# Kernel optimization log

Hardware: AMD Instinct MI355X
Metric: run time of the kernel (lower is better)

The kernel has to match this reference:

```python
import jax, jax.numpy as jnp
import numpy as np
from jax import lax

N_C = 2
T = 5
NE = 17   # equality constraints per (sample, t)
NV = 24   # variables per (sample, t): p(4), f(4), f_e(4), alpha1(2), alpha2(2), gamma(4), gamma_e(4)
ITERS = 400
B = 512

F_MASK = jnp.zeros((NV,), bool).at[4:8].set(True)     # L1-penalized coords (f)
NN_MASK = jnp.zeros((NV,), bool).at[12:24].set(True)  # nonneg coords (alpha1, alpha2, gamma, gamma_e)


def _conv(x, w, b):
    return lax.conv_general_dilated(x, w, (1, 1), 'VALID',
                                    dimension_numbers=('NCHW', 'OIHW', 'NCHW')) + b[None, :, None, None]


def _maxpool(x, k):
    return lax.reduce_window(x, -jnp.inf, lax.max, (1, 1, k, k), (1, 1, k, k), 'VALID')


def _encoder(img, cw1, cb1, cw2, cb2, w3, b3, w4, b4):
    h = jax.nn.relu(_maxpool(_conv(img, cw1, cb1), 2))   # (B,10,20,20)
    h = jax.nn.relu(_maxpool(_conv(h, cw2, cb2), 4))     # (B,20,4,4)
    h = h.reshape(h.shape[0], -1)                        # (B,320)
    h = jax.nn.relu(h @ w3.T + b3)                       # dropout is eval-mode identity
    return jax.nn.relu(h @ w4.T + b4)                    # (B,100)


def _mlp(h, w1, b1, w2, b2, w3, b3):
    h = jax.nn.relu(h @ w1.T + b1)  # dropout eval-mode identity
    h = jax.nn.relu(h @ w2.T + b2)
    return h @ w3.T + b3


def _build_Ab(r, ddr, fc, p_e, fc_e, v, p_r):
    # one (t)-slice: r(3), ddr(3), fc(8), p_e(4), fc_e(8), v(8), p_r(4) -> A(17,24), b(17)
    A = jnp.zeros((NE, NV))
    b = jnp.zeros((NE,))
    # force balance x: sum(f) + f_e0 + f_e1 = ddr0  (original f[:20] covers all 4 rows, f[20:] empty)
    A = A.at[0, 4:8].set(1.0).at[0, 8].set(1.0).at[0, 9].set(1.0)
    b = b.at[0].set(ddr[0])
    # force balance y: f_e2 + f_e3 = ddr1
    A = A.at[1, 10].set(1.0).at[1, 11].set(1.0)
    b = b.at[1].set(ddr[1])
    # torque balance
    A = A.at[2, 6].set(p_r[0] - r[0]).at[2, 4].set(-(p_r[2] - r[1]))
    A = A.at[2, 7].set(p_r[1] - r[0]).at[2, 5].set(-(p_r[3] - r[1]))
    A = A.at[2, 10].set(p_e[0] - r[0]).at[2, 8].set(-(p_e[2] - r[1]))
    A = A.at[2, 11].set(p_e[1] - r[0]).at[2, 9].set(-(p_e[3] - r[1]))
    b = b.at[2].set(ddr[2])
    for c in range(N_C):
        # p = alpha1*v_a + alpha2*v_b, alpha1+alpha2=1
        A = A.at[3 + 3 * c, c].set(1.0).at[3 + 3 * c, 12 + c].set(-v[2 * c]).at[3 + 3 * c, 14 + c].set(-v[2 * c + 2])
        A = A.at[4 + 3 * c, c + 2].set(1.0).at[4 + 3 * c, 12 + c].set(-v[2 * c + 1]).at[4 + 3 * c, 14 + c].set(-v[2 * c + 3])
        A = A.at[5 + 3 * c, 12 + c].set(1.0).at[5 + 3 * c, 14 + c].set(1.0)
        b = b.at[5 + 3 * c].set(1.0)
        # friction cone: f = gamma1*fc_a + gamma2*fc_b
        A = A.at[9 + 2 * c, 16 + c].set(fc[2 * c]).at[9 + 2 * c, 18 + c].set(fc[2 * c + 2]).at[9 + 2 * c, 4 + c].set(-1.0)
        A = A.at[10 + 2 * c, 16 + c].set(fc[2 * c + 1]).at[10 + 2 * c, 18 + c].set(fc[2 * c + 3]).at[10 + 2 * c, 6 + c].set(-1.0)
    # external force cones
    A = A.at[13, 20].set(fc_e[0]).at[13, 21].set(fc_e[2]).at[13, 8].set(-1.0)
    A = A.at[14, 20].set(fc_e[1]).at[14, 21].set(fc_e[3]).at[14, 10].set(-1.0)
    A = A.at[15, 22].set(fc_e[4]).at[15, 23].set(fc_e[6]).at[15, 9].set(-1.0)
    A = A.at[16, 22].set(fc_e[5]).at[16, 23].set(fc_e[7]).at[16, 11].set(-1.0)
    return A, b


def _specnorm(A):
    def body(i, u):
        u = A.T @ (A @ u)
        return u / (jnp.linalg.norm(u) + 1e-12)
    u = lax.fori_loop(0, 25, body, jnp.ones((A.shape[-1],), A.dtype))
    return jnp.linalg.norm(A @ u)


def _solve_lp(A, b):
    # batched: min ||f||_1  s.t.  A z = b,  z[nn] >= 0   via PDHG (Chambolle-Pock)
    P = A.shape[0]
    L = lax.stop_gradient(jax.vmap(_specnorm)(A))
    tau = (0.9 / (L + 1e-8))[:, None]
    sig = tau

    def step(carry, _):
        z, zb, y = carry
        y = y + sig * (jnp.einsum('pev,pv->pe', A, zb) - b)
        g = z - tau * jnp.einsum('pev,pe->pv', A, y)
        zn = jnp.where(F_MASK, jnp.sign(g) * jnp.maximum(jnp.abs(g) - tau, 0.0),
                       jnp.where(NN_MASK, jnp.maximum(g, 0.0), g))
        return (zn, 2.0 * zn - z, y), None

    z0 = jnp.zeros((P, NV))
    y0 = jnp.zeros((P, NE))
    (z, _, _), _ = lax.scan(step, (z0, z0, y0), None, length=ITERS)
    return z


def reference(xtraj, x, x_img, cw1, cb1, cw2, cb2, w3, b3, w4, b4,
              pw1, pb1, pw2, pb2, pw3, pb3, vw1, vb1, vw2, vb2, vw3, vb3):
    Bn = xtraj.shape[0]
    img = x_img.reshape(Bn, 1, 50, 50)
    e = _encoder(img, cw1, cb1, cw2, cb2, w3, b3, w4, b4)       # (B,100)
    h = jnp.concatenate([e, xtraj], axis=1)                     # (B,145)
    p_r = _mlp(h, pw1, pb1, pw2, pb2, pw3, pb3)                 # (B,20)
    v = _mlp(h, vw1, vb1, vw2, vb2, vw3, vb3)                   # (B,40)
    r = xtraj[:, :15].reshape(Bn, 3, T)
    ddr = xtraj[:, 30:45].reshape(Bn, 3, T)
    fc = x[:, 20:60].reshape(Bn, 8, T)
    p_e = x[:, 60:80].reshape(Bn, 4, T)
    fc_e = x[:, 80:120].reshape(Bn, 8, T)
    vM = v.reshape(Bn, 8, T)
    p_rM = p_r.reshape(Bn, 4, T)

    def flat(a):  # (B,d,T) -> (B*T, d)
        return jnp.swapaxes(a, 1, 2).reshape(Bn * T, a.shape[1])

    A, bvec = jax.vmap(_build_Ab)(flat(r), flat(ddr), flat(fc), flat(p_e), flat(fc_e), flat(vM), flat(p_rM))
    z = _solve_lp(A, bvec).reshape(Bn, T, NV)
    p = jnp.swapaxes(z[..., 0:4], 1, 2).reshape(Bn, 20)   # matches p.view(1,-1) C-order of (4,5)
    f = jnp.swapaxes(z[..., 4:8], 1, 2).reshape(Bn, 20)
    dp = p_r - x[:, 0:20]
    dv = v - x[:, 120:160]
    return 100.0 * jnp.concatenate([p, f, 10.0 * dp, 10.0 * dv], axis=1)  # (B,100)


def setup_inputs() -> dict:
    key = jax.random.key(0)
    ks = jax.random.split(key, 32)

    def rn(k, shape, s=0.05):
        return (s * jax.random.normal(k, shape)).astype(jnp.float32)

    return {
        'xtraj': rn(ks[0], (B, 45), 1.0),
        'x': rn(ks[1], (B, 160), 1.0),
        'x_img': rn(ks[2], (B, 2500), 1.0),
        'cw1': rn(ks[3], (10, 1, 11, 11)), 'cb1': rn(ks[4], (10,)),
        'cw2': rn(ks[5], (20, 10, 5, 5)), 'cb2': rn(ks[6], (20,)),
        'w3': rn(ks[7], (150, 320)), 'b3': rn(ks[8], (150,)),
        'w4': rn(ks[9], (100, 150)), 'b4': rn(ks[10], (100,)),
        'pw1': rn(ks[11], (100, 145)), 'pb1': rn(ks[12], (100,)),
        'pw2': rn(ks[13], (100, 100)), 'pb2': rn(ks[14], (100,)),
        'pw3': rn(ks[15], (20, 100)), 'pb3': rn(ks[16], (20,)),
        'vw1': rn(ks[17], (100, 145)), 'vb1': rn(ks[18], (100,)),
        'vw2': rn(ks[19], (100, 100)), 'vb2': rn(ks[20], (100,)),
        'vw3': rn(ks[21], (40, 100)), 'vb3': rn(ks[22], (40,)),
    }
```

## Files before the change

### kernel.cpp

```cpp
#include <hip/hip_runtime.h>

__device__ const signed char AZ_IDX[32][8] = {
    {4,5,6,7,8,9,0,0},{10,11,0,0,0,0,0,0},{4,5,6,7,8,9,10,11},
    {0,12,14,0,0,0,0,0},{2,12,14,0,0,0,0,0},{12,14,0,0,0,0,0,0},
    {1,13,15,0,0,0,0,0},{3,13,15,0,0,0,0,0},{13,15,0,0,0,0,0,0},
    {16,18,4,0,0,0,0,0},{16,18,6,0,0,0,0,0},{17,19,5,0,0,0,0,0},
    {17,19,7,0,0,0,0,0},{20,21,8,0,0,0,0,0},{20,21,10,0,0,0,0,0},
    {22,23,9,0,0,0,0,0},{22,23,11,0,0,0,0,0},
    {0},{0},{0},{0},{0},{0},{0},{0},{0},{0},{0},{0},{0},{0},{0}
};
__device__ const signed char AZ_SEL[32][8] = {
    {1,1,1,1,1,1,0,0},{1,1,0,0,0,0,0,0},{3,4,5,6,7,8,9,10},
    {1,11,13,0,0,0,0,0},{1,12,14,0,0,0,0,0},{1,1,0,0,0,0,0,0},
    {1,13,15,0,0,0,0,0},{1,14,16,0,0,0,0,0},{1,1,0,0,0,0,0,0},
    {17,19,2,0,0,0,0,0},{18,20,2,0,0,0,0,0},{19,21,2,0,0,0,0,0},
    {20,22,2,0,0,0,0,0},{23,25,2,0,0,0,0,0},{24,26,2,0,0,0,0,0},
    {27,29,2,0,0,0,0,0},{28,30,2,0,0,0,0,0},
    {0},{0},{0},{0},{0},{0},{0},{0},{0},{0},{0},{0},{0},{0},{0}
};
__device__ const signed char AT_IDX[32][3] = {
    {3,0,0},{6,0,0},{4,0,0},{7,0,0},
    {0,2,9},{0,2,11},{0,2,10},{0,2,12},{0,2,13},{0,2,15},{1,2,14},{1,2,16},
    {3,4,5},{6,7,8},{3,4,5},{6,7,8},
    {9,10,0},{11,12,0},{9,10,0},{11,12,0},
    {13,14,0},{13,14,0},{15,16,0},{15,16,0},
    {0},{0},{0},{0},{0},{0},{0},{0}
};
__device__ const signed char WBA[32] = {0,0,0,0, 4,4,4,4, 4,4,4,4, 0,0,0,0, 4,4,4,4, 8,8,8,8, 0,0,0,0,0,0,0,0};
__device__ const signed char WBB[32] = {12,12,12,12, 8,8,8,8, 8,8,8,8, 12,12,12,12, 16,16,16,16, 20,20,20,20, 0,0,0,0,0,0,0,0};
__device__ const signed char WBC[32] = {0,0,0,0, 16,16,16,16, 20,20,20,20, 0,0,0,0, 0,0,0,0, 0,0,0,0, 0,0,0,0,0,0,0,0};

#define LP_ITERS 400

__global__ __launch_bounds__(448) void net_kernel(
    const float* __restrict__ xtraj, const float* __restrict__ x,
    const float* __restrict__ x_img,
    const float* __restrict__ cw1, const float* __restrict__ cb1,
    const float* __restrict__ cw2, const float* __restrict__ cb2,
    const float* __restrict__ w3, const float* __restrict__ b3,
    const float* __restrict__ w4, const float* __restrict__ b4,
    const float* __restrict__ pw1, const float* __restrict__ pb1,
    const float* __restrict__ pw2, const float* __restrict__ pb2,
    const float* __restrict__ pw3, const float* __restrict__ pb3,
    const float* __restrict__ vw1, const float* __restrict__ vb1,
    const float* __restrict__ vw2, const float* __restrict__ vb2,
    const float* __restrict__ vw3, const float* __restrict__ vb3,
    float* __restrict__ out)
{
    const int b = blockIdx.x;
    const int tid = threadIdx.x;

    __shared__ __align__(16) float s_h1[4000];
    __shared__ __align__(16) float s_w2[5000];
    __shared__ __align__(16) float s_h2[320];
    __shared__ float s_hc[145];
    __shared__ float s_t1[152];
    __shared__ float s_m1[256];
    __shared__ float s_m2[256];

    float* Lb = s_h1;
    float* s_pr = Lb + 2285;
    float* s_vv = Lb + 2305;

    float* s_img = s_w2;

    {
        const float4* src = (const float4*)(x_img + (size_t)b * 2500);
        float4* dst = (float4*)s_img;
        for (int i = tid; i < 625; i += 448) dst[i] = src[i];
    }
    __syncthreads();

    if (tid < 400) {
        const int py = tid / 20, px = tid % 20;
        const int C = 2 * px;
        float acc0[10], acc1[10], acc2[10], acc3[10];
        #pragma unroll
        for (int oc = 0; oc < 10; ++oc) { acc0[oc] = 0.f; acc1[oc] = 0.f; acc2[oc] = 0.f; acc3[oc] = 0.f; }
        for (int r = 0; r < 12; ++r) {
            float v[12];
            #pragma unroll
            for (int j = 0; j < 6; ++j) {
                float2 t = *(const float2*)&s_img[(2 * py + r) * 50 + C + 2 * j];
                v[2 * j] = t.x; v[2 * j + 1] = t.y;
            }
            if (r < 11) {
                #pragma unroll
                for (int oc = 0; oc < 10; ++oc) {
                    #pragma unroll
                    for (int kx = 0; kx < 11; ++kx) {
                        float w0 = cw1[oc * 121 + r * 11 + kx];
                        acc0[oc] = fmaf(v[kx], w0, acc0[oc]);
                        acc1[oc] = fmaf(v[kx + 1], w0, acc1[oc]);
                    }
                }
            }
            if (r >= 1) {
                #pragma unroll
                for (int oc = 0; oc < 10; ++oc) {
                    #pragma unroll
                    for (int kx = 0; kx < 11; ++kx) {
                        float w1 = cw1[oc * 121 + (r - 1) * 11 + kx];
                        acc2[oc] = fmaf(v[kx], w1, acc2[oc]);
                        acc3[oc] = fmaf(v[kx + 1], w1, acc3[oc]);
                    }
                }
            }
        }
        #pragma unroll
        for (int oc = 0; oc < 10; ++oc) {
            float m = fmaxf(fmaxf(acc0[oc], acc1[oc]), fmaxf(acc2[oc], acc3[oc]));
            s_h1[oc * 400 + tid] = fmaxf(m + cb1[oc], 0.f);
        }
    }
    __syncthreads();

    {
        const float4* wsrc = (const float4*)cw2;
        float4* wdst = (float4*)s_w2;
        for (int i = tid; i < 1250; i += 448) wdst[i] = wsrc[i];
    }
    __syncthreads();

    if (tid < 320) {
        const int oc = tid >> 4, cell = tid & 15;
        const int R0 = (cell >> 2) * 4, C0 = (cell & 3) * 4;
        float acc[16];
        #pragma unroll
        for (int i = 0; i < 16; ++i) acc[i] = 0.f;
        for (int ic = 0; ic < 10; ++ic) {
            const float* hb = &s_h1[ic * 400];
            const float* wb = &s_w2[oc * 250 + ic * 25];
            float v[8][8];
            #pragma unroll
            for (int r = 0; r < 8; ++r) {
                float4 t0 = *(const float4*)&hb[(R0 + r) * 20 + C0];
                float4 t1 = *(const float4*)&hb[(R0 + r) * 20 + C0 + 4];
                v[r][0] = t0.x; v[r][1] = t0.y; v[r][2] = t0.z; v[r][3] = t0.w;
                v[r][4] = t1.x; v[r][5] = t1.y; v[r][6] = t1.z; v[r][7] = t1.w;
            }
            #pragma unroll
            for (int k = 0; k < 5; ++k) {
                #pragma unroll
                for (int kx = 0; kx < 5; ++kx) {
                    float wv = wb[k * 5 + kx];
                    #pragma unroll
                    for (int o = 0; o < 4; ++o) {
                        #pragma unroll
                        for (int cc = 0; cc < 4; ++cc)
                            acc[o * 4 + cc] = fmaf(v[o + k][cc + kx], wv, acc[o * 4 + cc]);
                    }
                }
            }
        }
        float m = acc[0];
        #pragma unroll
        for (int i = 1; i < 16; ++i) m = fmaxf(m, acc[i]);
        s_h2[tid] = fmaxf(m + cb2[oc], 0.f);
    }
    __syncthreads();

    if (tid < 150) {
        const float* w = w3 + tid * 320;
        float a0 = b3[tid], a1 = 0.f, a2 = 0.f, a3 = 0.f;
        for (int k = 0; k < 320; k += 4) {
            a0 = fmaf(s_h2[k],     w[k],     a0);
            a1 = fmaf(s_h2[k + 1], w[k + 1], a1);
            a2 = fmaf(s_h2[k + 2], w[k + 2], a2);
            a3 = fmaf(s_h2[k + 3], w[k + 3], a3);
        }
        s_t1[tid] = fmaxf((a0 + a1) + (a2 + a3), 0.f);
    }
    __syncthreads();

    if (tid < 100) {
        const float* w = w4 + tid * 150;
        float a0 = b4[tid], a1 = 0.f;
        for (int k = 0; k < 150; k += 2) {
            a0 = fmaf(s_t1[k],     w[k],     a0);
            a1 = fmaf(s_t1[k + 1], w[k + 1], a1);
        }
        s_hc[tid] = fmaxf(a0 + a1, 0.f);
    }
    if (tid >= 100 && tid < 145) s_hc[tid] = xtraj[b * 45 + (tid - 100)];
    __syncthreads();

    if (tid < 100) {
        const float* w = pw1 + tid * 145;
        float acc = pb1[tid];
        for (int k = 0; k < 145; ++k) acc = fmaf(s_hc[k], w[k], acc);
        s_m1[tid] = fmaxf(acc, 0.f);
    } else if (tid >= 128 && tid < 228) {
        int i = tid - 128;
        const float* w = vw1 + i * 145;
        float acc = vb1[i];
        for (int k = 0; k < 145; ++k) acc = fmaf(s_hc[k], w[k], acc);
        s_m1[tid] = fmaxf(acc, 0.f);
    }
    __syncthreads();

    if (tid < 100) {
        const float* w = pw2 + tid * 100;
        float acc = pb2[tid];
        for (int k = 0; k < 100; ++k) acc = fmaf(s_m1[k], w[k], acc);
        s_m2[tid] = fmaxf(acc, 0.f);
    } else if (tid >= 128 && tid < 228) {
        int i = tid - 128;
        const float* w = vw2 + i * 100;
        float acc = vb2[i];
        for (int k = 0; k < 100; ++k) acc = fmaf(s_m1[128 + k], w[k], acc);
        s_m2[tid] = fmaxf(acc, 0.f);
    }
    __syncthreads();

    if (tid < 20) {
        const float* w = pw3 + tid * 100;
        float acc = pb3[tid];
        for (int k = 0; k < 100; ++k) acc = fmaf(s_m2[k], w[k], acc);
        s_pr[tid] = acc;
        out[b * 100 + 40 + tid] = 1000.f * (acc - x[b * 160 + tid]);
    } else if (tid >= 128 && tid < 168) {
        int i = tid - 128;
        const float* w = vw3 + i * 100;
        float acc = vb3[i];
        for (int k = 0; k < 100; ++k) acc = fmaf(s_m2[128 + k], w[k], acc);
        s_vv[i] = acc;
        out[b * 100 + 60 + i] = 1000.f * (acc - x[b * 160 + 120 + i]);
    }
    __syncthreads();

    if (tid >= 160) return;
    const int t = tid >> 5;
    const int l = tid & 31;
    const float* xt = xtraj + b * 45;
    const float* xb = x + b * 160;

    float* val = Lb + t * 32;
    float* Ag  = Lb + 160 + t * 408;
    float* bg  = Lb + 2200 + t * 17;

    {
        float v_ = 0.f;
        if (l == 1) v_ = 1.f;
        else if (l == 2) v_ = -1.f;
        else if (l >= 3 && l <= 10) {
            float r0 = xt[t], r1 = xt[5 + t];
            switch (l) {
                case 3:  v_ = r1 - s_pr[10 + t]; break;
                case 4:  v_ = r1 - s_pr[15 + t]; break;
                case 5:  v_ = s_pr[0 + t] - r0;  break;
                case 6:  v_ = s_pr[5 + t] - r0;  break;
                case 7:  v_ = r1 - xb[60 + 10 + t]; break;
                case 8:  v_ = r1 - xb[60 + 15 + t]; break;
                case 9:  v_ = xb[60 + 0 + t] - r0;  break;
                default: v_ = xb[60 + 5 + t] - r0;  break;
            }
        }
        else if (l >= 11 && l <= 16) v_ = -s_vv[5 * (l - 11) + t];
        else if (l >= 17 && l <= 22) v_ = xb[20 + 5 * (l - 17) + t];
        else if (l >= 23 && l <= 30) v_ = xb[80 + 5 * (l - 23) + t];
        val[l] = v_;
    }
    for (int i = l; i < 408; i += 32) Ag[i] = 0.f;
    if (l < 17) {
        #pragma unroll
        for (int k = 0; k < 8; ++k) {
            int sel = AZ_SEL[l][k];
            if (sel != 0) Ag[l * 24 + (int)AZ_IDX[l][k]] = val[sel];
        }
        float bb = 0.f;
        if (l == 0) bb = xt[30 + t];
        else if (l == 1) bb = xt[35 + t];
        else if (l == 2) bb = xt[40 + t];
        else if (l == 5 || l == 8) bb = 1.f;
        bg[l] = bb;
    }

    const int bA = WBA[l], bB = WBB[l], bC = WBC[l];
    float cf[12];
    float cc = 0.f;
    #pragma unroll
    for (int k = 0; k < 12; ++k) cf[k] = 0.f;
    if (l < 24) {
        int e0 = AT_IDX[l][0], e1 = AT_IDX[l][1], e2 = AT_IDX[l][2];
        float a0 = Ag[e0 * 24 + l], a1 = Ag[e1 * 24 + l], a2 = Ag[e2 * 24 + l];
        cc = a0 * bg[e0] + a1 * bg[e1] + a2 * bg[e2];
        #pragma unroll
        for (int s = 0; s < 4; ++s)
            cf[s] = a0 * Ag[e0 * 24 + bA + s] + a1 * Ag[e1 * 24 + bA + s] + a2 * Ag[e2 * 24 + bA + s];
        #pragma unroll
        for (int s = 0; s < 4; ++s)
            cf[4 + s] = a0 * Ag[e0 * 24 + bB + s] + a1 * Ag[e1 * 24 + bB + s] + a2 * Ag[e2 * 24 + bB + s];
        if (l >= 4 && l < 12) {
            #pragma unroll
            for (int s = 0; s < 4; ++s)
                cf[8 + s] = a0 * Ag[e0 * 24 + bC + s] + a1 * Ag[e1 * 24 + bC + s] + a2 * Ag[e2 * 24 + bC + s];
        }
    }

    const bool isF  = (l >= 4 && l < 8);
    const bool isNN = (l >= 12);

    float* Zg = Lb + t * 32;

    #define WDOT(vA, vB, vC)                                                    \
        (((cf[0]*vA.x + cf[1]*vA.y) + (cf[2]*vA.z + cf[3]*vA.w)) +              \
         ((cf[4]*vB.x + cf[5]*vB.y) + (cf[6]*vB.z + cf[7]*vB.w)) +              \
         ((cf[8]*vC.x + cf[9]*vC.y) + (cf[10]*vC.z + cf[11]*vC.w)))

    float u = (l < 24) ? 1.f : 0.f;
    #pragma unroll 1
    for (int o = 0; o < 5; ++o) {
        #pragma unroll 1
        for (int ii = 0; ii < 5; ++ii) {
            Zg[l] = u;
            float4 vA = *(const float4*)(Zg + bA);
            float4 vB = *(const float4*)(Zg + bB);
            float4 vC = *(const float4*)(Zg + bC);
            u = WDOT(vA, vB, vC);
        }
        float s = u * u;
        s += __shfl_xor(s, 16, 32); s += __shfl_xor(s, 8, 32);
        s += __shfl_xor(s, 4, 32);  s += __shfl_xor(s, 2, 32);
        s += __shfl_xor(s, 1, 32);
        u = u / (sqrtf(s) + 1e-12f);
    }
    float tau;
    {
        Zg[l] = u;
        float4 vA = *(const float4*)(Zg + bA);
        float4 vB = *(const float4*)(Zg + bB);
        float4 vC = *(const float4*)(Zg + bC);
        float w = WDOT(vA, vB, vC);
        float s2 = u * w;
        s2 += __shfl_xor(s2, 16, 32); s2 += __shfl_xor(s2, 8, 32);
        s2 += __shfl_xor(s2, 4, 32);  s2 += __shfl_xor(s2, 2, 32);
        s2 += __shfl_xor(s2, 1, 32);
        tau = 0.9f / (sqrtf(fmaxf(s2, 0.f)) + 1e-8f);
    }

    const float t2 = tau * tau;
    #pragma unroll
    for (int k = 0; k < 12; ++k) cf[k] *= t2;
    const float cc2 = cc * t2;

    float zv = 0.f, zbv = 0.f, Q = 0.f;
    #pragma unroll 1
    for (int it = 0; it < LP_ITERS; ++it) {
        Zg[l] = zbv;
        float4 vA = *(const float4*)(Zg + bA);
        float4 vB = *(const float4*)(Zg + bB);
        float4 vC = *(const float4*)(Zg + bC);
        float Qm = Q - cc2;
        float s = WDOT(vA, vB, vC);
        Q = Qm + s;

        float gg = zv - Q;
        float cl = fminf(fmaxf(gg, -tau), tau);
        float st = gg - cl;
        float nn = fmaxf(gg, 0.f);
        float zn = isF ? st : (isNN ? nn : gg);
        zbv = fmaf(2.f, zn, -zv);
        zv = zn;
    }
    #undef WDOT

    {
        float* ob = out + b * 100;
        if (l < 4)      ob[l * 5 + t]            = 100.f * zv;
        else if (l < 8) ob[20 + (l - 4) * 5 + t] = 100.f * zv;
    }
}

extern "C" void kernel_launch(void* const* d_in, const int* in_sizes, int n_in,
                              void* d_out, int out_size, void* d_ws, size_t ws_size,
                              hipStream_t stream) {
    const float* xtraj = (const float*)d_in[0];
    const float* x     = (const float*)d_in[1];
    const float* x_img = (const float*)d_in[2];
    const float* cw1 = (const float*)d_in[3];
    const float* cb1 = (const float*)d_in[4];
    const float* cw2 = (const float*)d_in[5];
    const float* cb2 = (const float*)d_in[6];
    const float* w3  = (const float*)d_in[7];
    const float* b3  = (const float*)d_in[8];
    const float* w4  = (const float*)d_in[9];
    const float* b4  = (const float*)d_in[10];
    const float* pw1 = (const float*)d_in[11];
    const float* pb1 = (const float*)d_in[12];
    const float* pw2 = (const float*)d_in[13];
    const float* pb2 = (const float*)d_in[14];
    const float* pw3 = (const float*)d_in[15];
    const float* pb3 = (const float*)d_in[16];
    const float* vw1 = (const float*)d_in[17];
    const float* vb1 = (const float*)d_in[18];
    const float* vw2 = (const float*)d_in[19];
    const float* vb2 = (const float*)d_in[20];
    const float* vw3 = (const float*)d_in[21];
    const float* vb3 = (const float*)d_in[22];

    float* out = (float*)d_out;
    const int Bn = in_sizes[0] / 45;

    net_kernel<<<Bn, 448, 0, stream>>>(
        xtraj, x, x_img, cw1, cb1, cw2, cb2, w3, b3, w4, b4,
        pw1, pb1, pw2, pb2, pw3, pb3, vw1, vb1, vw2, vb2, vw3, vb3,
        out);
}
```

Measured before the change: 221.9 us.

## Compute dense layers with one wavefront per output row and shuffle reductions

Replaces the thread-per-output dense layers (encoder FC and both MLPs) with a wave-per-row scheme. Each of the 7 wavefronts takes output rows in turn, its lanes read consecutive weights so global loads coalesce, and partial sums are combined with cross-lane shuffles. This targets the uncoalesced strided weight reads and long serial dot products of the old mapping. In exchange it adds shuffle reduction overhead, and only 7 rows are processed at a time.

After: 315.7 us. 1.42x slower.

```diff
diff --git a/kernel.cpp b/kernel.cpp
--- a/kernel.cpp
+++ b/kernel.cpp
@@ -32,6 +32,19 @@
 
 #define LP_ITERS 400
 
+__device__ __forceinline__ float wave_dot(const float* __restrict__ wr,
+                                          const float* __restrict__ h,
+                                          int K, int lane) {
+    float acc = 0.f;
+    int j = lane;
+    for (; j + 64 <= K; j += 64) acc = fmaf(h[j], wr[j], acc);
+    if (j < K) acc = fmaf(h[j], wr[j], acc);
+    acc += __shfl_xor(acc, 32, 64); acc += __shfl_xor(acc, 16, 64);
+    acc += __shfl_xor(acc, 8, 64);  acc += __shfl_xor(acc, 4, 64);
+    acc += __shfl_xor(acc, 2, 64);  acc += __shfl_xor(acc, 1, 64);
+    return acc;
+}
+
 __global__ __launch_bounds__(448) void net_kernel(
     const float* __restrict__ xtraj, const float* __restrict__ x,
     const float* __restrict__ x_img,
@@ -49,6 +62,8 @@
 {
     const int b = blockIdx.x;
     const int tid = threadIdx.x;
+    const int wid = tid >> 6;
+    const int lane = tid & 63;
 
     __shared__ __align__(16) float s_h1[4000];
     __shared__ __align__(16) float s_w2[5000];
@@ -160,72 +175,57 @@
     }
     __syncthreads();
 
-    if (tid < 150) {
-        const float* w = w3 + tid * 320;
-        float a0 = b3[tid], a1 = 0.f, a2 = 0.f, a3 = 0.f;
-        for (int k = 0; k < 320; k += 4) {
-            a0 = fmaf(s_h2[k],     w[k],     a0);
-            a1 = fmaf(s_h2[k + 1], w[k + 1], a1);
-            a2 = fmaf(s_h2[k + 2], w[k + 2], a2);
-            a3 = fmaf(s_h2[k + 3], w[k + 3], a3);
-        }
-        s_t1[tid] = fmaxf((a0 + a1) + (a2 + a3), 0.f);
-    }
-    __syncthreads();
-
-    if (tid < 100) {
-        const float* w = w4 + tid * 150;
-        float a0 = b4[tid], a1 = 0.f;
-        for (int k = 0; k < 150; k += 2) {
-            a0 = fmaf(s_t1[k],     w[k],     a0);
-            a1 = fmaf(s_t1[k + 1], w[k + 1], a1);
-        }
-        s_hc[tid] = fmaxf(a0 + a1, 0.f);
-    }
-    if (tid >= 100 && tid < 145) s_hc[tid] = xtraj[b * 45 + (tid - 100)];
-    __syncthreads();
-
-    if (tid < 100) {
-        const float* w = pw1 + tid * 145;
-        float acc = pb1[tid];
-        for (int k = 0; k < 145; ++k) acc = fmaf(s_hc[k], w[k], acc);
-        s_m1[tid] = fmaxf(acc, 0.f);
-    } else if (tid >= 128 && tid < 228) {
-        int i = tid - 128;
-        const float* w = vw1 + i * 145;
-        float acc = vb1[i];
-        for (int k = 0; k < 145; ++k) acc = fmaf(s_hc[k], w[k], acc);
-        s_m1[tid] = fmaxf(acc, 0.f);
-    }
-    __syncthreads();
-
-    if (tid < 100) {
-        const float* w = pw2 + tid * 100;
-        float acc = pb2[tid];
-        for (int k = 0; k < 100; ++k) acc = fmaf(s_m1[k], w[k], acc);
-        s_m2[tid] = fmaxf(acc, 0.f);
-    } else if (tid >= 128 && tid < 228) {
-        int i = tid - 128;
-        const float* w = vw2 + i * 100;
-        float acc = vb2[i];
-        for (int k = 0; k < 100; ++k) acc = fmaf(s_m1[128 + k], w[k], acc);
-        s_m2[tid] = fmaxf(acc, 0.f);
-    }
-    __syncthreads();
-
-    if (tid < 20) {
-        const float* w = pw3 + tid * 100;
-        float acc = pb3[tid];
-        for (int k = 0; k < 100; ++k) acc = fmaf(s_m2[k], w[k], acc);
-        s_pr[tid] = acc;
-        out[b * 100 + 40 + tid] = 1000.f * (acc - x[b * 160 + tid]);
-    } else if (tid >= 128 && tid < 168) {
-        int i = tid - 128;
-        const float* w = vw3 + i * 100;
-        float acc = vb3[i];
-        for (int k = 0; k < 100; ++k) acc = fmaf(s_m2[128 + k], w[k], acc);
-        s_vv[i] = acc;
-        out[b * 100 + 60 + i] = 1000.f * (acc - x[b * 160 + 120 + i]);
+    for (int r = wid; r < 150; r += 7) {
+        float d = wave_dot(w3 + r * 320, s_h2, 320, lane);
+        if (lane == 0) s_t1[r] = fmaxf(d + b3[r], 0.f);
+    }
+    __syncthreads();
+
+    if (tid < 45) s_hc[100 + tid] = xtraj[b * 45 + tid];
+    for (int r = wid; r < 100; r += 7) {
+        float d = wave_dot(w4 + r * 150, s_t1, 150, lane);
+        if (lane == 0) s_hc[r] = fmaxf(d + b4[r], 0.f);
+    }
+    __syncthreads();
+
+    for (int r = wid; r < 200; r += 7) {
+        const bool isv = r >= 100;
+        const int o = isv ? r - 100 : r;
+        const float* W = isv ? vw1 : pw1;
+        const float* B = isv ? vb1 : pb1;
+        float d = wave_dot(W + o * 145, s_hc, 145, lane);
+        if (lane == 0) s_m1[(isv ? 128 : 0) + o] = fmaxf(d + B[o], 0.f);
+    }
+    __syncthreads();
+
+    for (int r = wid; r < 200; r += 7) {
+        const bool isv = r >= 100;
+        const int o = isv ? r - 100 : r;
+        const float* W = isv ? vw2 : pw2;
+        const float* B = isv ? vb2 : pb2;
+        const float* h = isv ? (s_m1 + 128) : s_m1;
+        float d = wave_dot(W + o * 100, h, 100, lane);
+        if (lane == 0) s_m2[(isv ? 128 : 0) + o] = fmaxf(d + B[o], 0.f);
+    }
+    __syncthreads();
+
+    for (int r = wid; r < 60; r += 7) {
+        const bool isv = r >= 20;
+        const int o = isv ? r - 20 : r;
+        const float* W = isv ? vw3 : pw3;
+        const float* B = isv ? vb3 : pb3;
+        const float* h = isv ? (s_m2 + 128) : s_m2;
+        float d = wave_dot(W + o * 100, h, 100, lane);
+        if (lane == 0) {
+            float acc = d + B[o];
+            if (isv) {
+                s_vv[o] = acc;
+                out[b * 100 + 60 + o] = 1000.f * (acc - x[b * 160 + 120 + o]);
+            } else {
+                s_pr[o] = acc;
+                out[b * 100 + 40 + o] = 1000.f * (acc - x[b * 160 + o]);
+            }
+        }
     }
     __syncthreads();
 
```
